# Optimization experiments

Hardware: AMD Instinct MI355X
Metric: run time of the kernel (lower is better)

Reference implementation:

```python
import jax, jax.numpy as jnp
import numpy as np

NUM_CLASSES = 21
GAMMA = 2.0
LAMBDA_WGT = 0.1
EPS = 1e-6
D, H, W = 256, 512, 512


def setup_inputs() -> dict:
    key = jax.random.key(0)
    k1, k2, k3, k4, k5 = jax.random.split(key, 5)
    # probabilities in (0,1); avoid exact 0 so log is finite
    y_pred = jax.random.uniform(k1, (NUM_CLASSES, H, W), dtype=jnp.float32, minval=1e-4, maxval=1.0)
    ycrf = jax.random.randint(k2, (H, W), 0, NUM_CLASSES, dtype=jnp.int32)
    yret = jax.random.randint(k3, (H, W), 0, NUM_CLASSES, dtype=jnp.int32)
    feature_map = jax.random.normal(k4, (D, H, W), dtype=jnp.float32)
    classifier_weight = jax.random.normal(k5, (NUM_CLASSES, D), dtype=jnp.float32)
    return {"y_pred": y_pred, "ycrf": ycrf, "yret": yret,
            "feature_map": feature_map, "classifier_weight": classifier_weight}


def reference(y_pred, ycrf, yret, feature_map, classifier_weight):
    C = NUM_CLASSES
    logp = jnp.log(y_pred)                                   # [C,H,W]
    # gather log p at the CRF label per pixel
    logp_crf = jnp.take_along_axis(logp, ycrf[None].astype(jnp.int32), axis=0)[0]  # [H,W]
    s = (ycrf == yret)                                       # pixels where ycrf==yret==c (s_class union)
    s_f = s.astype(logp.dtype)

    # ---- loss_ce: -sum_{p: ycrf==yret} log p[ycrf(p), p] / count ----
    denom_ce = jnp.sum(s_f)
    numer_ce = jnp.sum(jnp.where(s, logp_crf, 0.0))
    loss_ce = -numer_ce / denom_ce

    # ---- correlation map: 1 + cos(feature_map, w_c) along channel dim ----
    f_norm = jnp.maximum(jnp.sqrt(jnp.sum(feature_map * feature_map, axis=0)), EPS)   # [H,W]
    w_norm = jnp.maximum(jnp.sqrt(jnp.sum(classifier_weight * classifier_weight, axis=1)), EPS)  # [C]
    dots = jnp.einsum('dhw,cd->chw', feature_map, classifier_weight)                  # [C,H,W]
    corr = 1.0 + dots / (w_norm[:, None, None] * f_norm[None])                        # [C,H,W]

    # c* map = corr at the CRF label; original max includes an all-zeros extra row
    corr_star = jnp.take_along_axis(corr, ycrf[None].astype(jnp.int32), axis=0)[0]    # [H,W]
    corr_max = jnp.maximum(jnp.max(corr, axis=0), 0.0)                                # [H,W]
    conf = (corr_star / corr_max) ** GAMMA                                            # [H,W]

    # ---- loss_wce: per class i, sum over pixels NOT in s_i of conf * log p_i ----
    # each pixel appears (C - 1{ycrf==yret}) times in denom; numer excludes class ycrf when s holds
    denom_w = jnp.sum(conf * (C - s_f))
    numer_w = jnp.sum(conf * (jnp.sum(logp, axis=0) - s_f * logp_crf))
    loss_wce = -numer_w / denom_w

    return (loss_ce + LAMBDA_WGT * loss_wce, loss_ce, loss_wce)
```

## Files before the change

kernel.cpp:

```cpp
#include <hip/hip_runtime.h>
#include <math.h>

#define NCLS 21
#define DD   256
#define HWPIX (512*512)
#define HW2   (HWPIX/2)
#define EPSV  1e-6f

#define WT_STRIDE 24
#define WT_FLOATS (DD*WT_STRIDE)
#define THREADS 256
#define MAIN_BLOCKS (HW2/THREADS)
#define UND 8

typedef float __attribute__((ext_vector_type(2))) f2;
typedef float __attribute__((ext_vector_type(4))) f4;
typedef int   __attribute__((ext_vector_type(2))) i2;

__global__ void prep_weights(const float* __restrict__ w,
                             float* __restrict__ wt)
{
    __shared__ float inv_wn[NCLS];
    int tid = threadIdx.x;
    int wave = tid >> 6, lane = tid & 63;
    for (int c = wave; c < NCLS; c += 4) {
        float s = 0.f;
        #pragma unroll
        for (int k = 0; k < 4; ++k) {
            float v = w[c*DD + lane + 64*k];
            s = fmaf(v, v, s);
        }
        #pragma unroll
        for (int off = 32; off; off >>= 1) s += __shfl_xor(s, off, 64);
        if (lane == 0) inv_wn[c] = 1.0f / fmaxf(sqrtf(s), EPSV);
    }
    __syncthreads();
    for (int i = tid; i < NCLS*DD; i += THREADS) {
        int c = i / DD, d = i - c*DD;
        wt[d*WT_STRIDE + c] = w[i] * inv_wn[c];
    }
}

__global__ __launch_bounds__(THREADS, 2)
void main_kernel(const float* __restrict__ yp,
                 const int*   __restrict__ ycrf,
                 const int*   __restrict__ yret,
                 const float* __restrict__ fm,
                 const float* __restrict__ wt,
                 float* __restrict__ partials)
{
    __shared__ float lds_wt[WT_FLOATS];
    __shared__ float red[4][4];

    int tid = threadIdx.x;
    {
        const f4* src = (const f4*)wt;
        f4* dst = (f4*)lds_wt;
        #pragma unroll
        for (int i = 0; i < WT_FLOATS/4/THREADS; ++i)
            dst[i*THREADS + tid] = src[i*THREADS + tid];
    }
    __syncthreads();

    const int g = blockIdx.x * THREADS + tid;
    const f2* fm2 = (const f2*)fm;
    const f2* yp2 = (const f2*)yp;
    const i2* yc2 = (const i2*)ycrf;
    const i2* yr2 = (const i2*)yret;

    float dot0[NCLS], dot1[NCLS];
    float nn0 = 0.f, nn1 = 0.f;
    #pragma unroll
    for (int c = 0; c < NCLS; ++c) { dot0[c] = 0.f; dot1[c] = 0.f; }

    f2 v[UND];
    #pragma unroll
    for (int u = 0; u < UND; ++u)
        v[u] = __builtin_nontemporal_load(&fm2[u*HW2 + g]);

    for (int d0 = 0; d0 < DD; d0 += UND) {
        f2 nv[UND];
        if (d0 + UND < DD) {
            #pragma unroll
            for (int u = 0; u < UND; ++u)
                nv[u] = __builtin_nontemporal_load(&fm2[(d0 + UND + u)*HW2 + g]);
        }
        #pragma unroll
        for (int u = 0; u < UND; ++u) {
            float wreg[24];
            const f4* wr4 = (const f4*)&lds_wt[(d0 + u)*WT_STRIDE];
            #pragma unroll
            for (int i = 0; i < 6; ++i) ((f4*)wreg)[i] = wr4[i];
            float vx = v[u].x, vy = v[u].y;
            #pragma unroll
            for (int c = 0; c < NCLS; ++c) {
                dot0[c] = fmaf(vx, wreg[c], dot0[c]);
                dot1[c] = fmaf(vy, wreg[c], dot1[c]);
            }
            nn0 = fmaf(vx, vx, nn0);
            nn1 = fmaf(vy, vy, nn1);
        }
        #pragma unroll
        for (int u = 0; u < UND; ++u) v[u] = nv[u];
    }

    const i2 yc = yc2[g], yr = yr2[g];

    float inv_fn0 = 1.0f / fmaxf(sqrtf(nn0), EPSV);
    float inv_fn1 = 1.0f / fmaxf(sqrtf(nn1), EPSV);
    float cs0 = 0.f, cs1 = 0.f, cm0 = 0.f, cm1 = 0.f;
    #pragma unroll
    for (int c = 0; c < NCLS; ++c) {
        float c0 = fmaf(dot0[c], inv_fn0, 1.0f);
        float c1 = fmaf(dot1[c], inv_fn1, 1.0f);
        cm0 = fmaxf(cm0, c0);
        cm1 = fmaxf(cm1, c1);
        cs0 = (yc.x == c) ? c0 : cs0;
        cs1 = (yc.y == c) ? c1 : cs1;
    }
    float r0 = cs0 / cm0, r1 = cs1 / cm1;
    float conf0 = r0 * r0, conf1 = r1 * r1;

    f2 p[NCLS];
    #pragma unroll
    for (int c = 0; c < NCLS; ++c)
        p[c] = __builtin_nontemporal_load(&yp2[c*HW2 + g]);

    float slp0 = 0.f, slp1 = 0.f, lpc0 = 0.f, lpc1 = 0.f;
    #pragma unroll
    for (int c = 0; c < NCLS; ++c) {
        float l0 = __logf(p[c].x), l1 = __logf(p[c].y);
        slp0 += l0; slp1 += l1;
        lpc0 = (yc.x == c) ? l0 : lpc0;
        lpc1 = (yc.y == c) ? l1 : lpc1;
    }

    const bool s0 = (yc.x == yr.x), s1 = (yc.y == yr.y);
    float sl0 = s0 ? lpc0 : 0.f,  sl1 = s1 ? lpc1 : 0.f;
    float a_nce = sl0 + sl1;
    float a_dce = (s0 ? 1.f : 0.f) + (s1 ? 1.f : 0.f);
    float a_dw  = conf0 * ((float)NCLS - (s0 ? 1.f : 0.f))
                + conf1 * ((float)NCLS - (s1 ? 1.f : 0.f));
    float a_nw  = conf0 * (slp0 - sl0) + conf1 * (slp1 - sl1);

    #pragma unroll
    for (int off = 32; off; off >>= 1) {
        a_nce += __shfl_xor(a_nce, off, 64);
        a_dce += __shfl_xor(a_dce, off, 64);
        a_dw  += __shfl_xor(a_dw,  off, 64);
        a_nw  += __shfl_xor(a_nw,  off, 64);
    }
    int wave = tid >> 6, lane = tid & 63;
    if (lane == 0) { red[wave][0]=a_nce; red[wave][1]=a_dce; red[wave][2]=a_dw; red[wave][3]=a_nw; }
    __syncthreads();
    if (tid == 0) {
        #pragma unroll
        for (int i = 0; i < 4; ++i)
            partials[blockIdx.x*4 + i] = red[0][i] + red[1][i] + red[2][i] + red[3][i];
    }
}

__global__ void finalize(const float* __restrict__ partials, float* __restrict__ out)
{
    __shared__ float red[4][4];
    int tid = threadIdx.x;
    float s[4] = {0.f, 0.f, 0.f, 0.f};
    for (int b = tid; b < MAIN_BLOCKS; b += THREADS) {
        #pragma unroll
        for (int i = 0; i < 4; ++i) s[i] += partials[b*4 + i];
    }
    #pragma unroll
    for (int off = 32; off; off >>= 1) {
        #pragma unroll
        for (int i = 0; i < 4; ++i) s[i] += __shfl_xor(s[i], off, 64);
    }
    int wave = tid >> 6, lane = tid & 63;
    if (lane == 0) { red[wave][0]=s[0]; red[wave][1]=s[1]; red[wave][2]=s[2]; red[wave][3]=s[3]; }
    __syncthreads();
    if (tid == 0) {
        float nce = red[0][0]+red[1][0]+red[2][0]+red[3][0];
        float dce = red[0][1]+red[1][1]+red[2][1]+red[3][1];
        float dw  = red[0][2]+red[1][2]+red[2][2]+red[3][2];
        float nw  = red[0][3]+red[1][3]+red[2][3]+red[3][3];
        float ce  = -nce / dce;
        float wce = -nw  / dw;
        out[0] = ce + 0.1f * wce;
        out[1] = ce;
        out[2] = wce;
    }
}

extern "C" void kernel_launch(void* const* d_in, const int* in_sizes, int n_in,
                              void* d_out, int out_size, void* d_ws, size_t ws_size,
                              hipStream_t stream) {
    const float* y_pred = (const float*)d_in[0];
    const int*   ycrf   = (const int*)d_in[1];
    const int*   yret   = (const int*)d_in[2];
    const float* fmap   = (const float*)d_in[3];
    const float* cw     = (const float*)d_in[4];
    float* out = (float*)d_out;

    float* wt       = (float*)d_ws;
    float* partials = wt + WT_FLOATS;

    prep_weights<<<1, THREADS, 0, stream>>>(cw, wt);
    main_kernel<<<MAIN_BLOCKS, THREADS, 0, stream>>>(y_pred, ycrf, yret, fmap, wt, partials);
    finalize<<<1, THREADS, 0, stream>>>(partials, out);
}
```

Before: 76.37 us.

## Process one pixel per thread, read weights from global memory, raise occupancy

The main kernel now handles one pixel per thread instead of two, which halves the dot-product accumulator registers. It drops the LDS copy of the normalized weight matrix and reads the weights directly from global memory as uniform loads, which removes the per-block staging and barrier. Launch bounds go from 2 to 4 blocks per CU so more waves can hide memory latency. The cost is twice as many blocks, narrower per-thread loads, and weight reads that now depend on cache or scalar-load behaviour rather than LDS.

```diff
diff --git a/kernel.cpp b/kernel.cpp
--- a/kernel.cpp
+++ b/kernel.cpp
@@ -4,18 +4,15 @@
 #define NCLS 21
 #define DD   256
 #define HWPIX (512*512)
-#define HW2   (HWPIX/2)
 #define EPSV  1e-6f
 
 #define WT_STRIDE 24
 #define WT_FLOATS (DD*WT_STRIDE)
 #define THREADS 256
-#define MAIN_BLOCKS (HW2/THREADS)
+#define MAIN_BLOCKS (HWPIX/THREADS)
 #define UND 8
 
-typedef float __attribute__((ext_vector_type(2))) f2;
 typedef float __attribute__((ext_vector_type(4))) f4;
-typedef int   __attribute__((ext_vector_type(2))) i2;
 
 __global__ void prep_weights(const float* __restrict__ w,
                              float* __restrict__ wt)
@@ -35,13 +32,13 @@
         if (lane == 0) inv_wn[c] = 1.0f / fmaxf(sqrtf(s), EPSV);
     }
     __syncthreads();
-    for (int i = tid; i < NCLS*DD; i += THREADS) {
-        int c = i / DD, d = i - c*DD;
-        wt[d*WT_STRIDE + c] = w[i] * inv_wn[c];
+    for (int i = tid; i < DD*WT_STRIDE; i += THREADS) {
+        int d = i / WT_STRIDE, c = i - d*WT_STRIDE;
+        wt[i] = (c < NCLS) ? w[c*DD + d] * inv_wn[c] : 0.f;
     }
 }
 
-__global__ __launch_bounds__(THREADS, 2)
+__global__ __launch_bounds__(THREADS, 4)
 void main_kernel(const float* __restrict__ yp,
                  const int*   __restrict__ ycrf,
                  const int*   __restrict__ yret,
@@ -49,99 +46,76 @@
                  const float* __restrict__ wt,
                  float* __restrict__ partials)
 {
-    __shared__ float lds_wt[WT_FLOATS];
     __shared__ float red[4][4];
 
-    int tid = threadIdx.x;
-    {
-        const f4* src = (const f4*)wt;
-        f4* dst = (f4*)lds_wt;
-        #pragma unroll
-        for (int i = 0; i < WT_FLOATS/4/THREADS; ++i)
-            dst[i*THREADS + tid] = src[i*THREADS + tid];
-    }
-    __syncthreads();
+    const int tid = threadIdx.x;
+    const int g = blockIdx.x * THREADS + tid;
 
-    const int g = blockIdx.x * THREADS + tid;
-    const f2* fm2 = (const f2*)fm;
-    const f2* yp2 = (const f2*)yp;
-    const i2* yc2 = (const i2*)ycrf;
-    const i2* yr2 = (const i2*)yret;
+    float dot[NCLS];
+    float nn = 0.f;
+    #pragma unroll
+    for (int c = 0; c < NCLS; ++c) dot[c] = 0.f;
 
-    float dot0[NCLS], dot1[NCLS];
-    float nn0 = 0.f, nn1 = 0.f;
-    #pragma unroll
-    for (int c = 0; c < NCLS; ++c) { dot0[c] = 0.f; dot1[c] = 0.f; }
-
-    f2 v[UND];
+    float v[UND];
     #pragma unroll
     for (int u = 0; u < UND; ++u)
-        v[u] = __builtin_nontemporal_load(&fm2[u*HW2 + g]);
+        v[u] = __builtin_nontemporal_load(&fm[u*HWPIX + g]);
 
     for (int d0 = 0; d0 < DD; d0 += UND) {
-        f2 nv[UND];
+        float nv[UND];
         if (d0 + UND < DD) {
             #pragma unroll
             for (int u = 0; u < UND; ++u)
-                nv[u] = __builtin_nontemporal_load(&fm2[(d0 + UND + u)*HW2 + g]);
+                nv[u] = __builtin_nontemporal_load(&fm[(d0 + UND + u)*HWPIX + g]);
         }
         #pragma unroll
         for (int u = 0; u < UND; ++u) {
+            const f4* wr = (const f4*)(wt + (d0 + u)*WT_STRIDE);
             float wreg[24];
-            const f4* wr4 = (const f4*)&lds_wt[(d0 + u)*WT_STRIDE];
             #pragma unroll
-            for (int i = 0; i < 6; ++i) ((f4*)wreg)[i] = wr4[i];
-            float vx = v[u].x, vy = v[u].y;
+            for (int i = 0; i < 6; ++i) ((f4*)wreg)[i] = wr[i];
+            float vx = v[u];
             #pragma unroll
-            for (int c = 0; c < NCLS; ++c) {
-                dot0[c] = fmaf(vx, wreg[c], dot0[c]);
-                dot1[c] = fmaf(vy, wreg[c], dot1[c]);
-            }
-            nn0 = fmaf(vx, vx, nn0);
-            nn1 = fmaf(vy, vy, nn1);
+            for (int c = 0; c < NCLS; ++c)
+                dot[c] = fmaf(vx, wreg[c], dot[c]);
+            nn = fmaf(vx, vx, nn);
         }
         #pragma unroll
         for (int u = 0; u < UND; ++u) v[u] = nv[u];
     }
 
-    const i2 yc = yc2[g], yr = yr2[g];
+    const int yc = ycrf[g], yr = yret[g];
 
-    float inv_fn0 = 1.0f / fmaxf(sqrtf(nn0), EPSV);
-    float inv_fn1 = 1.0f / fmaxf(sqrtf(nn1), EPSV);
-    float cs0 = 0.f, cs1 = 0.f, cm0 = 0.f, cm1 = 0.f;
+    float inv_fn = 1.0f / fmaxf(sqrtf(nn), EPSV);
+    float cs = 0.f, cm = 0.f;
     #pragma unroll
     for (int c = 0; c < NCLS; ++c) {
-        float c0 = fmaf(dot0[c], inv_fn0, 1.0f);
-        float c1 = fmaf(dot1[c], inv_fn1, 1.0f);
-        cm0 = fmaxf(cm0, c0);
-        cm1 = fmaxf(cm1, c1);
-        cs0 = (yc.x == c) ? c0 : cs0;
-        cs1 = (yc.y == c) ? c1 : cs1;
+        float cv = fmaf(dot[c], inv_fn, 1.0f);
+        cm = fmaxf(cm, cv);
+        cs = (yc == c) ? cv : cs;
     }
-    float r0 = cs0 / cm0, r1 = cs1 / cm1;
-    float conf0 = r0 * r0, conf1 = r1 * r1;
+    float r = cs / cm;
+    float conf = r * r;
 
-    f2 p[NCLS];
+    float p[NCLS];
     #pragma unroll
     for (int c = 0; c < NCLS; ++c)
-        p[c] = __builtin_nontemporal_load(&yp2[c*HW2 + g]);
+        p[c] = __builtin_nontemporal_load(&yp[c*HWPIX + g]);
 
-    float slp0 = 0.f, slp1 = 0.f, lpc0 = 0.f, lpc1 = 0.f;
+    float slp = 0.f, lpc = 0.f;
     #pragma unroll
     for (int c = 0; c < NCLS; ++c) {
-        float l0 = __logf(p[c].x), l1 = __logf(p[c].y);
-        slp0 += l0; slp1 += l1;
-        lpc0 = (yc.x == c) ? l0 : lpc0;
-        lpc1 = (yc.y == c) ? l1 : lpc1;
+        float l = __logf(p[c]);
+        slp += l;
+        lpc = (yc == c) ? l : lpc;
     }
 
-    const bool s0 = (yc.x == yr.x), s1 = (yc.y == yr.y);
-    float sl0 = s0 ? lpc0 : 0.f,  sl1 = s1 ? lpc1 : 0.f;
-    float a_nce = sl0 + sl1;
-    float a_dce = (s0 ? 1.f : 0.f) + (s1 ? 1.f : 0.f);
-    float a_dw  = conf0 * ((float)NCLS - (s0 ? 1.f : 0.f))
-                + conf1 * ((float)NCLS - (s1 ? 1.f : 0.f));
-    float a_nw  = conf0 * (slp0 - sl0) + conf1 * (slp1 - sl1);
+    const bool s = (yc == yr);
+    float sl = s ? lpc : 0.f;
+    float a_nce = sl;
+    float a_dce = s ? 1.f : 0.f;
+    float a_dw  = conf * ((float)NCLS - (s ? 1.f : 0.f));
+    float a_nw  = conf * (slp - sl);
 
     #pragma unroll
     for (int off = 32; off; off >>= 1) {
```

After: 75.37 us. About the same (-1.3%).

## Fuse finalize into main kernel via last-block reduction; read weights directly from global

Applied to the files above, without the earlier changes.

Removes the separate finalize launch by having the last block to finish (found with an atomic counter) reduce all partials and write the outputs. The LDS staging of the normalized weights is dropped, so each thread reads them straight from global memory (cached, wave-uniform addresses), and prep_weights is spread over one block per class, which also resets the counter. Nontemporal loads on the feature map and predictions become ordinary loads. The trade-off is scalar/global loads in the inner FMA loop instead of LDS reads, plus the atomic and fence cost at the end of every block.

```diff
diff --git a/kernel.cpp b/kernel.cpp
--- a/kernel.cpp
+++ b/kernel.cpp
@@ -18,27 +18,24 @@
 typedef int   __attribute__((ext_vector_type(2))) i2;
 
 __global__ void prep_weights(const float* __restrict__ w,
-                             float* __restrict__ wt)
+                             float* __restrict__ wt,
+                             unsigned* __restrict__ counter)
 {
-    __shared__ float inv_wn[NCLS];
-    int tid = threadIdx.x;
-    int wave = tid >> 6, lane = tid & 63;
-    for (int c = wave; c < NCLS; c += 4) {
-        float s = 0.f;
-        #pragma unroll
-        for (int k = 0; k < 4; ++k) {
-            float v = w[c*DD + lane + 64*k];
-            s = fmaf(v, v, s);
-        }
-        #pragma unroll
-        for (int off = 32; off; off >>= 1) s += __shfl_xor(s, off, 64);
-        if (lane == 0) inv_wn[c] = 1.0f / fmaxf(sqrtf(s), EPSV);
-    }
-    __syncthreads();
-    for (int i = tid; i < NCLS*DD; i += THREADS) {
-        int c = i / DD, d = i - c*DD;
-        wt[d*WT_STRIDE + c] = w[i] * inv_wn[c];
-    }
+    __shared__ float warr[4];
+    __shared__ float inv_s;
+    const int c = blockIdx.x, d = threadIdx.x;
+    if (c == 0 && d == 0) *counter = 0u;
+
+    float v = w[c*DD + d];
+    float s = v * v;
+    #pragma unroll
+    for (int off = 32; off; off >>= 1) s += __shfl_xor(s, off, 64);
+    int wave = d >> 6, lane = d & 63;
+    if (lane == 0) warr[wave] = s;
+    __syncthreads();
+    if (d == 0) inv_s = 1.0f / fmaxf(sqrtf(warr[0]+warr[1]+warr[2]+warr[3]), EPSV);
+    __syncthreads();
+    wt[d*WT_STRIDE + c] = v * inv_s;
 }
 
 __global__ __launch_bounds__(THREADS, 2)
@@ -47,21 +44,14 @@
                  const int*   __restrict__ yret,
                  const float* __restrict__ fm,
                  const float* __restrict__ wt,
-                 float* __restrict__ partials)
+                 float* __restrict__ partials,
+                 unsigned* __restrict__ counter,
+                 float* __restrict__ out)
 {
-    __shared__ float lds_wt[WT_FLOATS];
     __shared__ float red[4][4];
-
-    int tid = threadIdx.x;
-    {
-        const f4* src = (const f4*)wt;
-        f4* dst = (f4*)lds_wt;
-        #pragma unroll
-        for (int i = 0; i < WT_FLOATS/4/THREADS; ++i)
-            dst[i*THREADS + tid] = src[i*THREADS + tid];
-    }
-    __syncthreads();
-
+    __shared__ bool amlast;
+
+    const int tid = threadIdx.x;
     const int g = blockIdx.x * THREADS + tid;
     const f2* fm2 = (const f2*)fm;
     const f2* yp2 = (const f2*)yp;
@@ -76,21 +66,21 @@
     f2 v[UND];
     #pragma unroll
     for (int u = 0; u < UND; ++u)
-        v[u] = __builtin_nontemporal_load(&fm2[u*HW2 + g]);
+        v[u] = fm2[u*HW2 + g];
 
     for (int d0 = 0; d0 < DD; d0 += UND) {
         f2 nv[UND];
         if (d0 + UND < DD) {
             #pragma unroll
             for (int u = 0; u < UND; ++u)
-                nv[u] = __builtin_nontemporal_load(&fm2[(d0 + UND + u)*HW2 + g]);
+                nv[u] = fm2[(d0 + UND + u)*HW2 + g];
         }
         #pragma unroll
         for (int u = 0; u < UND; ++u) {
+            const f4* wr = (const f4*)(wt + (d0 + u)*WT_STRIDE);
             float wreg[24];
-            const f4* wr4 = (const f4*)&lds_wt[(d0 + u)*WT_STRIDE];
             #pragma unroll
-            for (int i = 0; i < 6; ++i) ((f4*)wreg)[i] = wr4[i];
+            for (int i = 0; i < 6; ++i) ((f4*)wreg)[i] = wr[i];
             float vx = v[u].x, vy = v[u].y;
             #pragma unroll
             for (int c = 0; c < NCLS; ++c) {
@@ -124,7 +114,7 @@
     f2 p[NCLS];
     #pragma unroll
     for (int c = 0; c < NCLS; ++c)
-        p[c] = __builtin_nontemporal_load(&yp2[c*HW2 + g]);
+        p[c] = yp2[c*HW2 + g];
 
     float slp0 = 0.f, slp1 = 0.f, lpc0 = 0.f, lpc1 = 0.f;
     #pragma unroll
@@ -157,36 +147,42 @@
         #pragma unroll
         for (int i = 0; i < 4; ++i)
             partials[blockIdx.x*4 + i] = red[0][i] + red[1][i] + red[2][i] + red[3][i];
-    }
-}
-
-__global__ void finalize(const float* __restrict__ partials, float* __restrict__ out)
-{
-    __shared__ float red[4][4];
-    int tid = threadIdx.x;
-    float s[4] = {0.f, 0.f, 0.f, 0.f};
-    for (int b = tid; b < MAIN_BLOCKS; b += THREADS) {
-        #pragma unroll
-        for (int i = 0; i < 4; ++i) s[i] += partials[b*4 + i];
-    }
-    #pragma unroll
-    for (int off = 32; off; off >>= 1) {
-        #pragma unroll
-        for (int i = 0; i < 4; ++i) s[i] += __shfl_xor(s[i], off, 64);
-    }
-    int wave = tid >> 6, lane = tid & 63;
-    if (lane == 0) { red[wave][0]=s[0]; red[wave][1]=s[1]; red[wave][2]=s[2]; red[wave][3]=s[3]; }
-    __syncthreads();
-    if (tid == 0) {
-        float nce = red[0][0]+red[1][0]+red[2][0]+red[3][0];
-        float dce = red[0][1]+red[1][1]+red[2][1]+red[3][1];
-        float dw  = red[0][2]+red[1][2]+red[2][2]+red[3][2];
-        float nw  = red[0][3]+red[1][3]+red[2][3]+red[3][3];
-        float ce  = -nce / dce;
-        float wce = -nw  / dw;
-        out[0] = ce + 0.1f * wce;
-        out[1] = ce;
-        out[2] = wce;
+        __threadfence();
+        unsigned old = atomicAdd(counter, 1u);
+        amlast = (old == (unsigned)(MAIN_BLOCKS - 1));
+    }
+    __syncthreads();
+
+    if (amlast) {
+        __threadfence();
+        float t0=0.f, t1=0.f, t2=0.f, t3=0.f;
+        for (int b = tid; b < MAIN_BLOCKS; b += THREADS) {
+            t0 += partials[b*4 + 0];
+            t1 += partials[b*4 + 1];
+            t2 += partials[b*4 + 2];
+            t3 += partials[b*4 + 3];
+        }
+        #pragma unroll
+        for (int off = 32; off; off >>= 1) {
+            t0 += __shfl_xor(t0, off, 64);
+            t1 += __shfl_xor(t1, off, 64);
+            t2 += __shfl_xor(t2, off, 64);
+            t3 += __shfl_xor(t3, off, 64);
+        }
+        __syncthreads();
+        if (lane == 0) { red[wave][0]=t0; red[wave][1]=t1; red[wave][2]=t2; red[wave][3]=t3; }
+        __syncthreads();
+        if (tid == 0) {
+            float nce = red[0][0]+red[1][0]+red[2][0]+red[3][0];
+            float dce = red[0][1]+red[1][1]+red[2][1]+red[3][1];
+            float dw  = red[0][2]+red[1][2]+red[2][2]+red[3][2];
+            float nw  = red[0][3]+red[1][3]+red[2][3]+red[3][3];
+            float ce  = -nce / dce;
+            float wce = -nw  / dw;
+            out[0] = ce + 0.1f * wce;
+            out[1] = ce;
+            out[2] = wce;
+        }
     }
 }
 
@@ -200,10 +196,11 @@
     const float* cw     = (const float*)d_in[4];
     float* out = (float*)d_out;
 
-    float* wt       = (float*)d_ws;
-    float* partials = wt + WT_FLOATS;
-
-    prep_weights<<<1, THREADS, 0, stream>>>(cw, wt);
-    main_kernel<<<MAIN_BLOCKS, THREADS, 0, stream>>>(y_pred, ycrf, yret, fmap, wt, partials);
-    finalize<<<1, THREADS, 0, stream>>>(partials, out);
+    float*    wt       = (float*)d_ws;
+    float*    partials = wt + WT_FLOATS;
+    unsigned* counter  = (unsigned*)(partials + MAIN_BLOCKS*4);
+
+    prep_weights<<<NCLS, THREADS, 0, stream>>>(cw, wt, counter);
+    main_kernel<<<MAIN_BLOCKS, THREADS, 0, stream>>>(y_pred, ycrf, yret, fmap, wt,
+                                                     partials, counter, out);
 }
```

After: 94.03 us. +23.1%, slower.

## Read weights from global/scalar cache, double-buffer feature loads, parallelize weight prep

Applied to the files above, without the earlier changes.

Removes the 24KB LDS staging of normalized weights in the main kernel; weights are read directly from global memory at uniform addresses, which the compiler can serve with scalar loads. The feature-map prefetch becomes two alternating register buffers so loads for the next chunk are issued while the current chunk is computed. Weight prep now runs one block per class instead of a single block. This drops the LDS fill and the barrier at block start, but each thread now reads the weights through the cache and carries more live registers.

```diff
diff --git a/kernel.cpp b/kernel.cpp
--- a/kernel.cpp
+++ b/kernel.cpp
@@ -20,25 +20,19 @@
 __global__ void prep_weights(const float* __restrict__ w,
                              float* __restrict__ wt)
 {
-    __shared__ float inv_wn[NCLS];
-    int tid = threadIdx.x;
-    int wave = tid >> 6, lane = tid & 63;
-    for (int c = wave; c < NCLS; c += 4) {
-        float s = 0.f;
-        #pragma unroll
-        for (int k = 0; k < 4; ++k) {
-            float v = w[c*DD + lane + 64*k];
-            s = fmaf(v, v, s);
-        }
-        #pragma unroll
-        for (int off = 32; off; off >>= 1) s += __shfl_xor(s, off, 64);
-        if (lane == 0) inv_wn[c] = 1.0f / fmaxf(sqrtf(s), EPSV);
-    }
-    __syncthreads();
-    for (int i = tid; i < NCLS*DD; i += THREADS) {
-        int c = i / DD, d = i - c*DD;
-        wt[d*WT_STRIDE + c] = w[i] * inv_wn[c];
-    }
+    __shared__ float warr[4];
+    __shared__ float inv_s;
+    const int c = blockIdx.x, d = threadIdx.x;
+    float v = w[c*DD + d];
+    float s = v * v;
+    #pragma unroll
+    for (int off = 32; off; off >>= 1) s += __shfl_xor(s, off, 64);
+    int wave = d >> 6, lane = d & 63;
+    if (lane == 0) warr[wave] = s;
+    __syncthreads();
+    if (d == 0) inv_s = 1.0f / fmaxf(sqrtf(warr[0]+warr[1]+warr[2]+warr[3]), EPSV);
+    __syncthreads();
+    wt[d*WT_STRIDE + c] = v * inv_s;
 }
 
 __global__ __launch_bounds__(THREADS, 2)
@@ -49,19 +43,9 @@
                  const float* __restrict__ wt,
                  float* __restrict__ partials)
 {
-    __shared__ float lds_wt[WT_FLOATS];
     __shared__ float red[4][4];
 
-    int tid = threadIdx.x;
-    {
-        const f4* src = (const f4*)wt;
-        f4* dst = (f4*)lds_wt;
-        #pragma unroll
-        for (int i = 0; i < WT_FLOATS/4/THREADS; ++i)
-            dst[i*THREADS + tid] = src[i*THREADS + tid];
-    }
-    __syncthreads();
-
+    const int tid = threadIdx.x;
     const int g = blockIdx.x * THREADS + tid;
     const f2* fm2 = (const f2*)fm;
     const f2* yp2 = (const f2*)yp;
@@ -73,36 +57,48 @@
     #pragma unroll
     for (int c = 0; c < NCLS; ++c) { dot0[c] = 0.f; dot1[c] = 0.f; }
 
-    f2 v[UND];
+    f2 vA[UND], vB[UND];
     #pragma unroll
     for (int u = 0; u < UND; ++u)
-        v[u] = __builtin_nontemporal_load(&fm2[u*HW2 + g]);
-
-    for (int d0 = 0; d0 < DD; d0 += UND) {
-        f2 nv[UND];
-        if (d0 + UND < DD) {
+        vA[u] = __builtin_nontemporal_load(&fm2[u*HW2 + g]);
+    #pragma unroll
+    for (int u = 0; u < UND; ++u)
+        vB[u] = __builtin_nontemporal_load(&fm2[(UND + u)*HW2 + g]);
+
+    #define COMPUTE(VREG, DBASE)                                            \
+        do {                                                                \
+            _Pragma("unroll")                                               \
+            for (int u = 0; u < UND; ++u) {                                 \
+                const f4* wr = (const f4*)(wt + ((DBASE) + u)*WT_STRIDE);   \
+                float wreg[24];                                             \
+                _Pragma("unroll")                                           \
+                for (int i = 0; i < 6; ++i) ((f4*)wreg)[i] = wr[i];         \
+                float vx = VREG[u].x, vy = VREG[u].y;                       \
+                _Pragma("unroll")                                           \
+                for (int c = 0; c < NCLS; ++c) {                            \
+                    dot0[c] = fmaf(vx, wreg[c], dot0[c]);                   \
+                    dot1[c] = fmaf(vy, wreg[c], dot1[c]);                   \
+                }                                                           \
+                nn0 = fmaf(vx, vx, nn0);                                    \
+                nn1 = fmaf(vy, vy, nn1);                                    \
+            }                                                               \
+        } while (0)
+
+    for (int d0 = 0; d0 < DD; d0 += 2*UND) {
+        COMPUTE(vA, d0);
+        if (d0 + 2*UND < DD) {
             #pragma unroll
             for (int u = 0; u < UND; ++u)
-                nv[u] = __builtin_nontemporal_load(&fm2[(d0 + UND + u)*HW2 + g]);
+                vA[u] = __builtin_nontemporal_load(&fm2[(d0 + 2*UND + u)*HW2 + g]);
         }
-        #pragma unroll
-        for (int u = 0; u < UND; ++u) {
-            float wreg[24];
-            const f4* wr4 = (const f4*)&lds_wt[(d0 + u)*WT_STRIDE];
+        COMPUTE(vB, d0 + UND);
+        if (d0 + 3*UND < DD) {
             #pragma unroll
-            for (int i = 0; i < 6; ++i) ((f4*)wreg)[i] = wr4[i];
-            float vx = v[u].x, vy = v[u].y;
-            #pragma unroll
-            for (int c = 0; c < NCLS; ++c) {
-                dot0[c] = fmaf(vx, wreg[c], dot0[c]);
-                dot1[c] = fmaf(vy, wreg[c], dot1[c]);
-            }
-            nn0 = fmaf(vx, vx, nn0);
-            nn1 = fmaf(vy, vy, nn1);
+            for (int u = 0; u < UND; ++u)
+                vB[u] = __builtin_nontemporal_load(&fm2[(d0 + 3*UND + u)*HW2 + g]);
         }
-        #pragma unroll
-        for (int u = 0; u < UND; ++u) v[u] = nv[u];
-    }
+    }
+    #undef COMPUTE
 
     const i2 yc = yc2[g], yr = yr2[g];
 
@@ -203,7 +199,7 @@
     float* wt       = (float*)d_ws;
     float* partials = wt + WT_FLOATS;
 
-    prep_weights<<<1, THREADS, 0, stream>>>(cw, wt);
+    prep_weights<<<NCLS, THREADS, 0, stream>>>(cw, wt);
     main_kernel<<<MAIN_BLOCKS, THREADS, 0, stream>>>(y_pred, ycrf, yret, fmap, wt, partials);
     finalize<<<1, THREADS, 0, stream>>>(partials, out);
 }
```

Result: slower. 160.0 us (+109.5%).
